# Kernel optimization log

Measured on AMD Instinct MI355X. Metric: run time of the kernel, lower is better.

The kernel has to match this reference:

```python
import jax, jax.numpy as jnp
import numpy as np

N = 100000
E = 1600000
IN_DIM = 128
HID_DIM = 64
OUT_DIM = 1


def setup_inputs() -> dict:
    key = jax.random.key(0)
    k = jax.random.split(key, 8)
    x = jax.random.normal(k[0], (N, IN_DIM), dtype=jnp.float32)
    edge_index = jax.random.randint(k[1], (2, E), 0, N, dtype=jnp.int64)
    # GCNConv glorot-style weights, zero biases
    W1 = jax.random.normal(k[2], (IN_DIM, HID_DIM), dtype=jnp.float32) / np.sqrt(IN_DIM)
    b1 = jnp.zeros((HID_DIM,), dtype=jnp.float32)
    W2 = jax.random.normal(k[3], (HID_DIM, 2), dtype=jnp.float32) / np.sqrt(HID_DIM)
    b2 = jnp.zeros((2,), dtype=jnp.float32)
    Wc = jax.random.normal(k[4], (2, OUT_DIM), dtype=jnp.float32) / np.sqrt(2.0)
    bc = jnp.zeros((OUT_DIM,), dtype=jnp.float32)
    return {"x": x, "edge_index": edge_index, "W1": W1, "b1": b1,
            "W2": W2, "b2": b2, "Wc": Wc, "bc": bc}


def _gcn_conv(x, W, b, row, col, norm, n_nodes):
    """PyG GCNConv: transform, then normalized scatter-add aggregation."""
    h = x @ W                      # [N, out] transform BEFORE propagation
    msgs = h[row] * norm[:, None]  # gather from source nodes, scale
    out = jax.ops.segment_sum(msgs, col, num_segments=n_nodes)  # scatter to targets
    return out + b


def _prep_edges(edge_index, n_nodes):
    # add self-loops (PyG default add_self_loops=True)
    loops = jnp.arange(n_nodes, dtype=edge_index.dtype)
    row = jnp.concatenate([edge_index[0], loops])
    col = jnp.concatenate([edge_index[1], loops])
    # symmetric normalization deg^{-1/2} on both endpoints (edge weight 1)
    deg = jax.ops.segment_sum(jnp.ones_like(col, dtype=jnp.float32), col,
                              num_segments=n_nodes)
    dis = jnp.where(deg > 0, jax.lax.rsqrt(deg), 0.0)
    norm = dis[row] * dis[col]
    return row, col, norm


def reference(x, edge_index, W1, b1, W2, b2, Wc, bc):
    n_nodes = x.shape[0]
    row, col, norm = _prep_edges(edge_index, n_nodes)
    h = jnp.tanh(_gcn_conv(x, W1, b1, row, col, norm, n_nodes))
    emb = jnp.tanh(_gcn_conv(h, W2, b2, row, col, norm, n_nodes))
    return jax.nn.sigmoid(emb @ Wc + bc)  # [N, 1]
```

## Files before the change

### kernel.cpp

```cpp
#include <hip/hip_runtime.h>
#include <math.h>

#define IN_DIM 128
#define HID 64
#define NPB 128
#define NPB_SH 7
#define CAP 4096
#define CHUNK 2048
#define CPT 2

typedef __attribute__((ext_vector_type(8))) short bf16x8;
typedef __attribute__((ext_vector_type(4))) float f32x4;
typedef __attribute__((ext_vector_type(4))) _Float16 f16x4;

static __device__ inline short f2bf(float f) {
    unsigned u = __float_as_uint(f);
    u += 0x7fff + ((u >> 16) & 1);
    return (short)(u >> 16);
}

__device__ __forceinline__ void scanExcl1024(const unsigned* in, unsigned* out,
                                             int m, int t, unsigned* wsum) {
    unsigned v = (t < m) ? in[t] : 0u;
    unsigned incl = v;
    int lane = t & 63;
#pragma unroll
    for (int off = 1; off < 64; off <<= 1) {
        unsigned u = __shfl_up(incl, off, 64);
        if (lane >= off) incl += u;
    }
    if (lane == 63) wsum[t >> 6] = incl;
    __syncthreads();
    if (t < 16) {
        unsigned w = wsum[t];
        unsigned winc = w;
#pragma unroll
        for (int off = 1; off < 16; off <<= 1) {
            unsigned u = __shfl_up(winc, off, 64);
            if (t >= off) winc += u;
        }
        wsum[t] = winc - w;
    }
    __syncthreads();
    if (t < m) out[t] = incl - v + wsum[t >> 6];
}

__global__ void k_packW(const float* __restrict__ W1, ushort* __restrict__ W1p) {
    int idx = blockIdx.x * 256 + threadIdx.x;
    int i = idx & 7, lane = (idx >> 3) & 63, fb = (idx >> 9) & 3, kc = (idx >> 11) & 3;
    int k = kc * 32 + (lane >> 4) * 8 + i;
    int f = fb * 16 + (lane & 15);
    W1p[idx] = (ushort)f2bf(W1[k * HID + f]);
}

__global__ void __launch_bounds__(1024) k_binpairs(
        const int* __restrict__ row, const int* __restrict__ col,
        unsigned* __restrict__ pairsA, unsigned short* __restrict__ chk,
        int E, int nbuk) {
    __shared__ unsigned cntL[1024];
    __shared__ unsigned offs[1024];
    __shared__ unsigned wsum[16];
    __shared__ unsigned stage[CHUNK];
    int t = threadIdx.x;
    int base = blockIdx.x * CHUNK;
    int cc = min(CHUNK, E - base);

    cntL[t] = 0;
    __syncthreads();

    unsigned myPk[CPT], myR[CPT];
    int myB[CPT];
#pragma unroll
    for (int i = 0; i < CPT; ++i) {
        int j = i * 1024 + t;
        myB[i] = -1;
        if (j < cc) {
            int r = row[base + j], c = col[base + j];
            int b = c >> NPB_SH;
            myR[i] = atomicAdd(&cntL[b], 1u);
            myPk[i] = (unsigned)r | ((unsigned)(c & (NPB - 1)) << 24);
            myB[i] = b;
        }
    }
    __syncthreads();
    scanExcl1024(cntL, offs, nbuk, t, wsum);
    __syncthreads();
#pragma unroll
    for (int i = 0; i < CPT; ++i)
        if (myB[i] >= 0) stage[offs[myB[i]] + myR[i]] = myPk[i];
    __syncthreads();
    for (int j = t; j < cc; j += 1024) pairsA[base + j] = stage[j];
    size_t rb = (size_t)blockIdx.x * (nbuk + 1);
    if (t < nbuk) chk[rb + t] = (unsigned short)offs[t];
    if (t == 0) chk[rb + nbuk] = (unsigned short)cc;
}

__global__ void __launch_bounds__(1024) k_sort(
        const unsigned* __restrict__ pairsA, const unsigned short* __restrict__ chk,
        unsigned* __restrict__ pairs2, unsigned* __restrict__ offsG,
        float* __restrict__ dis, int nblk, int nbuk, int n) {
    __shared__ unsigned cntB[1024];
    __shared__ unsigned baseB[1024];
    __shared__ unsigned wsum[16];
    __shared__ unsigned stage[CAP];
    __shared__ unsigned sorted[CAP];
    __shared__ unsigned cntN[NPB];
    __shared__ unsigned offsN[NPB];
    __shared__ unsigned cur[NPB];
    __shared__ unsigned totS;
    int t = threadIdx.x, b = blockIdx.x;

    unsigned s = 0, cntT = 0;
    if (t < nblk) {
        size_t rb = (size_t)t * (nbuk + 1);
        s = chk[rb + b];
        cntT = chk[rb + b + 1] - s;
    }
    cntB[t] = cntT;
    __syncthreads();
    scanExcl1024(cntB, baseB, nblk, t, wsum);
    __syncthreads();
    if (t == 0) totS = baseB[nblk - 1] + cntB[nblk - 1];
    if (t < NPB) cntN[t] = 0;
    if (t < nblk && cntT) {
        unsigned dst = baseB[t];
        const unsigned* sp = pairsA + (size_t)t * CHUNK + s;
        for (unsigned k = 0; k < cntT; ++k)
            if (dst + k < CAP) stage[dst + k] = sp[k];
    }
    __syncthreads();
    int cbt = (int)min(totS, (unsigned)CAP);
    for (int i = t; i < cbt; i += 1024) atomicAdd(&cntN[stage[i] >> 24], 1u);
    __syncthreads();
    scanExcl1024(cntN, offsN, NPB, t, wsum);
    __syncthreads();
    if (t < NPB) cur[t] = offsN[t];
    __syncthreads();
    for (int i = t; i < cbt; i += 1024) {
        unsigned pk = stage[i];
        sorted[atomicAdd(&cur[pk >> 24], 1u)] = pk;
    }
    __syncthreads();
    int cb4 = (cbt + 3) >> 2;
    for (int i = t; i < cb4; i += 1024)
        ((uint4*)(pairs2 + (size_t)b * CAP))[i] = ((const uint4*)sorted)[i];
    if (t <= NPB) offsG[(size_t)b * (NPB + 1) + t] = (t < NPB) ? offsN[t] : (unsigned)cbt;
    int nd = b * NPB + t;
    if (t < NPB && nd < n) dis[nd] = rsqrtf((float)(cntN[t] + 1));
}

__global__ void __launch_bounds__(256) k_gemm1(const float* __restrict__ x,
                                               const ushort* __restrict__ W1p,
                                               const float* __restrict__ dis,
                                               _Float16* __restrict__ h1s, int n) {
    int t = threadIdx.x, wave = t >> 6, lane = t & 63;
    int nb = blockIdx.x * 64 + wave * 16;
    int arow = nb + (lane & 15);
    int g = lane >> 4;
    const bf16x8* Wp = (const bf16x8*)W1p;

    f32x4 acc0 = {0.f, 0.f, 0.f, 0.f}, acc1 = acc0, acc2 = acc0, acc3 = acc0;

#pragma unroll
    for (int kc = 0; kc < 4; ++kc) {
        bf16x8 a;
        if (arow < n) {
            const float4* xp = (const float4*)(x + (size_t)arow * IN_DIM + kc * 32 + g * 8);
            float4 x0 = xp[0], x1 = xp[1];
            a[0] = f2bf(x0.x); a[1] = f2bf(x0.y); a[2] = f2bf(x0.z); a[3] = f2bf(x0.w);
            a[4] = f2bf(x1.x); a[5] = f2bf(x1.y); a[6] = f2bf(x1.z); a[7] = f2bf(x1.w);
        } else {
            for (int i = 0; i < 8; ++i) a[i] = 0;
        }
        acc0 = __builtin_amdgcn_mfma_f32_16x16x32_bf16(a, Wp[(kc * 4 + 0) * 64 + lane], acc0, 0, 0, 0);
        acc1 = __builtin_amdgcn_mfma_f32_16x16x32_bf16(a, Wp[(kc * 4 + 1) * 64 + lane], acc1, 0, 0, 0);
        acc2 = __builtin_amdgcn_mfma_f32_16x16x32_bf16(a, Wp[(kc * 4 + 2) * 64 + lane], acc2, 0, 0, 0);
        acc3 = __builtin_amdgcn_mfma_f32_16x16x32_bf16(a, Wp[(kc * 4 + 3) * 64 + lane], acc3, 0, 0, 0);
    }

    int c = lane & 15, rbase = g * 4;
    float dn[4];
    int nd[4];
#pragma unroll
    for (int r = 0; r < 4; ++r) {
        nd[r] = nb + rbase + r;
        dn[r] = (nd[r] < n) ? dis[nd[r]] : 0.f;
    }
#define EPI(FB, ACC)                                                          \
    {                                                                         \
        int f = FB * 16 + c;                                                  \
        _Pragma("unroll") for (int r = 0; r < 4; ++r) {                       \
            if (nd[r] < n)                                                    \
                h1s[(size_t)nd[r] * HID + f] = (_Float16)(ACC[r] * dn[r]);    \
        }                                                                     \
    }
    EPI(0, acc0) EPI(1, acc1) EPI(2, acc2) EPI(3, acc3)
#undef EPI
}

__global__ void __launch_bounds__(512, 8) k_gather1(
        const unsigned* __restrict__ pairs2, const unsigned* __restrict__ offsG,
        const _Float16* __restrict__ h1s, const float* __restrict__ dis,
        const float* __restrict__ b1, const float* __restrict__ W2,
        float* __restrict__ es, int n) {
    __shared__ unsigned sorted[CAP];
    __shared__ unsigned offs[NPB + 1];
    int t = threadIdx.x, b = blockIdx.x;
    if (t <= NPB) offs[t] = offsG[(size_t)b * (NPB + 1) + t];
    __syncthreads();
    int cbt = (int)offs[NPB];
    int cb4 = (cbt + 3) >> 2;
    for (int i = t; i < cb4; i += 512)
        ((uint4*)sorted)[i] = ((const uint4*)(pairs2 + (size_t)b * CAP))[i];
    __syncthreads();

    int wave = t >> 6, lane = t & 63;
    int grp = lane >> 4, sub = lane & 15;
    float4 bb  = *(const float4*)(b1 + sub * 4);
    float4 w01 = *(const float4*)(W2 + sub * 8);
    float4 w23 = *(const float4*)(W2 + sub * 8 + 4);
    for (int it = 0; it < 16; ++it) {
        int dl = wave * 16 + it;
        int nd = b * NPB + dl;
        if (nd >= n) break;
        int p0 = (int)offs[dl] + grp, p1 = (int)offs[dl + 1];
        float a0 = 0.f, a1 = 0.f, a2 = 0.f, a3 = 0.f;
        for (int pp = p0; pp < p1; pp += 32) {
            f16x4 hacc = {(_Float16)0, (_Float16)0, (_Float16)0, (_Float16)0};
#pragma unroll
            for (int u = 0; u < 8; ++u) {
                int p = pp + u * 4;
                if (p < p1) {
                    unsigned srcn = sorted[p] & 0xFFFFFFu;
                    hacc += *(const f16x4*)(h1s + (size_t)srcn * HID + sub * 4);
                }
            }
            a0 += (float)hacc[0]; a1 += (float)hacc[1];
            a2 += (float)hacc[2]; a3 += (float)hacc[3];
        }
        a0 += __shfl_xor(a0, 16); a0 += __shfl_xor(a0, 32);
        a1 += __shfl_xor(a1, 16); a1 += __shfl_xor(a1, 32);
        a2 += __shfl_xor(a2, 16); a2 += __shfl_xor(a2, 32);
        a3 += __shfl_xor(a3, 16); a3 += __shfl_xor(a3, 32);
        f16x4 sv = *(const f16x4*)(h1s + (size_t)nd * HID + sub * 4);
        a0 += (float)sv[0]; a1 += (float)sv[1]; a2 += (float)sv[2]; a3 += (float)sv[3];
        float d = dis[nd];
        float v0 = tanhf(fmaf(a0, d, bb.x));
        float v1 = tanhf(fmaf(a1, d, bb.y));
        float v2 = tanhf(fmaf(a2, d, bb.z));
        float v3 = tanhf(fmaf(a3, d, bb.w));
        float s0 = v0 * w01.x + v1 * w01.z + v2 * w23.x + v3 * w23.z;
        float s1 = v0 * w01.y + v1 * w01.w + v2 * w23.y + v3 * w23.w;
        s0 += __shfl_xor(s0, 1); s1 += __shfl_xor(s1, 1);
        s0 += __shfl_xor(s0, 2); s1 += __shfl_xor(s1, 2);
        s0 += __shfl_xor(s0, 4); s1 += __shfl_xor(s1, 4);
        s0 += __shfl_xor(s0, 8); s1 += __shfl_xor(s1, 8);
        if (lane == 0) {
            es[nd * 2 + 0] = s0 * d;
            es[nd * 2 + 1] = s1 * d;
        }
    }
}

__global__ void __launch_bounds__(128) k_pass2b(
        const unsigned* __restrict__ pairs2, const unsigned* __restrict__ offsG,
        const float* __restrict__ es, const float* __restrict__ dis,
        const float* __restrict__ b2, const float* __restrict__ Wc,
        const float* __restrict__ bc, float* __restrict__ out, int n) {
    int t = threadIdx.x, b = blockIdx.x;
    int nd = b * NPB + t;
    if (nd >= n) return;
    const unsigned* seg = pairs2 + (size_t)b * CAP;
    int p0 = (int)offsG[(size_t)b * (NPB + 1) + t];
    int p1 = (int)offsG[(size_t)b * (NPB + 1) + t + 1];
    float2 self = *(const float2*)(es + (size_t)nd * 2);
    float a0 = self.x, a1 = self.y;
    for (int p = p0; p < p1; ++p) {
        unsigned srcn = seg[p] & 0xFFFFFFu;
        float2 v = *(const float2*)(es + (size_t)srcn * 2);
        a0 += v.x; a1 += v.y;
    }
    float d = dis[nd];
    float e0 = tanhf(fmaf(a0, d, b2[0]));
    float e1 = tanhf(fmaf(a1, d, b2[1]));
    float z = fmaf(e0, Wc[0], fmaf(e1, Wc[1], bc[0]));
    out[nd] = 1.f / (1.f + expf(-z));
}

extern "C" void kernel_launch(void* const* d_in, const int* in_sizes, int n_in,
                              void* d_out, int out_size, void* d_ws, size_t ws_size,
                              hipStream_t stream) {
    const float* x  = (const float*)d_in[0];
    const int*   ei = (const int*)d_in[1];
    const float* W1 = (const float*)d_in[2];
    const float* b1 = (const float*)d_in[3];
    const float* W2 = (const float*)d_in[4];
    const float* b2 = (const float*)d_in[5];
    const float* Wc = (const float*)d_in[6];
    const float* bc = (const float*)d_in[7];

    const int n = in_sizes[0] / IN_DIM;
    const int E = in_sizes[1] / 2;
    const int* row = ei;
    const int* col = ei + E;
    const int nbuk = (n + NPB - 1) / NPB;
    const int nblk = (E + CHUNK - 1) / CHUNK;

    char* w = (char*)d_ws;
    auto alloc = [&](size_t bytes) {
        char* p = w;
        w += (bytes + 511) & ~(size_t)511;
        return p;
    };
    unsigned*       pairsA = (unsigned*)alloc((size_t)nblk * CHUNK * 4);
    unsigned short* chk    = (unsigned short*)alloc((size_t)nblk * (nbuk + 1) * 2);
    unsigned*       pairs2 = (unsigned*)alloc((size_t)nbuk * CAP * 4);
    unsigned*       offsG  = (unsigned*)alloc((size_t)nbuk * (NPB + 1) * 4);
    float*          dis    = (float*)alloc((size_t)n * 4);
    ushort*         W1p    = (ushort*)alloc(16 * 64 * 8 * 2);
    _Float16*       h1s    = (_Float16*)alloc((size_t)n * HID * 2);
    float*          es     = (float*)alloc((size_t)n * 2 * 4);

    k_packW   <<<32, 256, 0, stream>>>(W1, W1p);
    k_binpairs<<<nblk, 1024, 0, stream>>>(row, col, pairsA, chk, E, nbuk);
    k_sort    <<<nbuk, 1024, 0, stream>>>(pairsA, chk, pairs2, offsG, dis,
                                          nblk, nbuk, n);
    k_gemm1   <<<(n + 63) / 64, 256, 0, stream>>>(x, W1p, dis, h1s, n);
    k_gather1 <<<nbuk, 512, 0, stream>>>(pairs2, offsG, h1s, dis, b1, W2, es, n);
    k_pass2b  <<<nbuk, 128, 0, stream>>>(pairs2, offsG, es, dis, b2, Wc, bc,
                                         (float*)d_out, n);
}
```

Measured before the change: 125.2 us.

## Split gather1 into 64-node blocks and use 16-byte f16x8 row loads

```diff
diff --git a/kernel.cpp b/kernel.cpp
--- a/kernel.cpp
+++ b/kernel.cpp
@@ -12,6 +12,7 @@
 typedef __attribute__((ext_vector_type(8))) short bf16x8;
 typedef __attribute__((ext_vector_type(4))) float f32x4;
 typedef __attribute__((ext_vector_type(4))) _Float16 f16x4;
+typedef __attribute__((ext_vector_type(8))) _Float16 f16x8;
 
 static __device__ inline short f2bf(float f) {
     unsigned u = __float_as_uint(f);
@@ -198,63 +199,86 @@
 #undef EPI
 }
 
-__global__ void __launch_bounds__(512, 8) k_gather1(
+__global__ void __launch_bounds__(256, 8) k_gather1(
         const unsigned* __restrict__ pairs2, const unsigned* __restrict__ offsG,
         const _Float16* __restrict__ h1s, const float* __restrict__ dis,
         const float* __restrict__ b1, const float* __restrict__ W2,
         float* __restrict__ es, int n) {
-    __shared__ unsigned sorted[CAP];
-    __shared__ unsigned offs[NPB + 1];
-    int t = threadIdx.x, b = blockIdx.x;
-    if (t <= NPB) offs[t] = offsG[(size_t)b * (NPB + 1) + t];
-    __syncthreads();
-    int cbt = (int)offs[NPB];
-    int cb4 = (cbt + 3) >> 2;
-    for (int i = t; i < cb4; i += 512)
-        ((uint4*)sorted)[i] = ((const uint4*)(pairs2 + (size_t)b * CAP))[i];
+    __shared__ unsigned sortedL[CAP];
+    __shared__ unsigned offsL[65];
+    int t = threadIdx.x;
+    int nb0 = blockIdx.x * 64;
+    int b = nb0 >> NPB_SH;
+    int dl0 = nb0 & (NPB - 1);
+    if (t <= 64) offsL[t] = offsG[(size_t)b * (NPB + 1) + dl0 + t];
+    __syncthreads();
+    int o0 = (int)offsL[0], o1 = (int)offsL[64];
+    for (int i = t; i < o1 - o0; i += 256)
+        sortedL[i] = pairs2[(size_t)b * CAP + o0 + i];
     __syncthreads();
 
     int wave = t >> 6, lane = t & 63;
-    int grp = lane >> 4, sub = lane & 15;
-    float4 bb  = *(const float4*)(b1 + sub * 4);
-    float4 w01 = *(const float4*)(W2 + sub * 8);
-    float4 w23 = *(const float4*)(W2 + sub * 8 + 4);
+    int grp = lane >> 3, sub = lane & 7;
+    float4 bbA = *(const float4*)(b1 + sub * 8);
+    float4 bbB = *(const float4*)(b1 + sub * 8 + 4);
+    float4 wA = *(const float4*)(W2 + sub * 16);
+    float4 wB = *(const float4*)(W2 + sub * 16 + 4);
+    float4 wC = *(const float4*)(W2 + sub * 16 + 8);
+    float4 wD = *(const float4*)(W2 + sub * 16 + 12);
+
     for (int it = 0; it < 16; ++it) {
         int dl = wave * 16 + it;
-        int nd = b * NPB + dl;
+        int nd = nb0 + dl;
         if (nd >= n) break;
-        int p0 = (int)offs[dl] + grp, p1 = (int)offs[dl + 1];
-        float a0 = 0.f, a1 = 0.f, a2 = 0.f, a3 = 0.f;
+        int p0 = (int)offsL[dl] + grp, p1 = (int)offsL[dl + 1];
+        float a0 = 0.f, a1 = 0.f, a2 = 0.f, a3 = 0.f,
+              a4 = 0.f, a5 = 0.f, a6 = 0.f, a7 = 0.f;
         for (int pp = p0; pp < p1; pp += 32) {
-            f16x4 hacc = {(_Float16)0, (_Float16)0, (_Float16)0, (_Float16)0};
-#pragma unroll
-            for (int u = 0; u < 8; ++u) {
-                int p = pp + u * 4;
+            f16x8 hacc = {0, 0, 0, 0, 0, 0, 0, 0};
+#pragma unroll
+            for (int u = 0; u < 4; ++u) {
+                int p = pp + u * 8;
                 if (p < p1) {
-                    unsigned srcn = sorted[p] & 0xFFFFFFu;
-                    hacc += *(const f16x4*)(h1s + (size_t)srcn * HID + sub * 4);
+                    unsigned srcn = sortedL[p - o0] & 0xFFFFFFu;
+                    hacc += *(const f16x8*)(h1s + (size_t)srcn * HID + sub * 8);
                 }
             }
             a0 += (float)hacc[0]; a1 += (float)hacc[1];
             a2 += (float)hacc[2]; a3 += (float)hacc[3];
-        }
-        a0 += __shfl_xor(a0, 16); a0 += __shfl_xor(a0, 32);
-        a1 += __shfl_xor(a1, 16); a1 += __shfl_xor(a1, 32);
-        a2 += __shfl_xor(a2, 16); a2 += __shfl_xor(a2, 32);
-        a3 += __shfl_xor(a3, 16); a3 += __shfl_xor(a3, 32);
-        f16x4 sv = *(const f16x4*)(h1s + (size_t)nd * HID + sub * 4);
+            a4 += (float)hacc[4]; a5 += (float)hacc[5];
+            a6 += (float)hacc[6]; a7 += (float)hacc[7];
+        }
+        a0 += __shfl_xor(a0, 8);  a1 += __shfl_xor(a1, 8);
+        a2 += __shfl_xor(a2, 8);  a3 += __shfl_xor(a3, 8);
+        a4 += __shfl_xor(a4, 8);  a5 += __shfl_xor(a5, 8);
+        a6 += __shfl_xor(a6, 8);  a7 += __shfl_xor(a7, 8);
+        a0 += __shfl_xor(a0, 16); a1 += __shfl_xor(a1, 16);
+        a2 += __shfl_xor(a2, 16); a3 += __shfl_xor(a3, 16);
+        a4 += __shfl_xor(a4, 16); a5 += __shfl_xor(a5, 16);
+        a6 += __shfl_xor(a6, 16); a7 += __shfl_xor(a7, 16);
+        a0 += __shfl_xor(a0, 32); a1 += __shfl_xor(a1, 32);
+        a2 += __shfl_xor(a2, 32); a3 += __shfl_xor(a3, 32);
+        a4 += __shfl_xor(a4, 32); a5 += __shfl_xor(a5, 32);
+        a6 += __shfl_xor(a6, 32); a7 += __shfl_xor(a7, 32);
+        f16x8 sv = *(const f16x8*)(h1s + (size_t)nd * HID + sub * 8);
         a0 += (float)sv[0]; a1 += (float)sv[1]; a2 += (float)sv[2]; a3 += (float)sv[3];
+        a4 += (float)sv[4]; a5 += (float)sv[5]; a6 += (float)sv[6]; a7 += (float)sv[7];
         float d = dis[nd];
-        float v0 = tanhf(fmaf(a0, d, bb.x));
-        float v1 = tanhf(fmaf(a1, d, bb.y));
-        float v2 = tanhf(fmaf(a2, d, bb.z));
-        float v3 = tanhf(fmaf(a3, d, bb.w));
-        float s0 = v0 * w01.x + v1 * w01.z + v2 * w23.x + v3 * w23.z;
-        float s1 = v0 * w01.y + v1 * w01.w + v2 * w23.y + v3 * w23.w;
+        float v0 = tanhf(fmaf(a0, d, bbA.x));
+        float v1 = tanhf(fmaf(a1, d, bbA.y));
+        float v2 = tanhf(fmaf(a2, d, bbA.z));
+        float v3 = tanhf(fmaf(a3, d, bbA.w));
+        float v4 = tanhf(fmaf(a4, d, bbB.x));
+        float v5 = tanhf(fmaf(a5, d, bbB.y));
+        float v6 = tanhf(fmaf(a6, d, bbB.z));
+        float v7 = tanhf(fmaf(a7, d, bbB.w));
+        float s0 = v0 * wA.x + v1 * wA.z + v2 * wB.x + v3 * wB.z
+                 + v4 * wC.x + v5 * wC.z + v6 * wD.x + v7 * wD.z;
+        float s1 = v0 * wA.y + v1 * wA.w + v2 * wB.y + v3 * wB.w
+                 + v4 * wC.y + v5 * wC.w + v6 * wD.y + v7 * wD.w;
         s0 += __shfl_xor(s0, 1); s1 += __shfl_xor(s1, 1);
         s0 += __shfl_xor(s0, 2); s1 += __shfl_xor(s1, 2);
         s0 += __shfl_xor(s0, 4); s1 += __shfl_xor(s1, 4);
-        s0 += __shfl_xor(s0, 8); s1 += __shfl_xor(s1, 8);
         if (lane == 0) {
             es[nd * 2 + 0] = s0 * d;
             es[nd * 2 + 1] = s1 * d;
@@ -326,7 +350,7 @@
     k_sort    <<<nbuk, 1024, 0, stream>>>(pairsA, chk, pairs2, offsG, dis,
                                           nblk, nbuk, n);
     k_gemm1   <<<(n + 63) / 64, 256, 0, stream>>>(x, W1p, dis, h1s, n);
-    k_gather1 <<<nbuk, 512, 0, stream>>>(pairs2, offsG, h1s, dis, b1, W2, es, n);
+    k_gather1 <<<(n + 63) / 64, 256, 0, stream>>>(pairs2, offsG, h1s, dis, b1, W2, es, n);
     k_pass2b  <<<nbuk, 128, 0, stream>>>(pairs2, offsG, es, dis, b2, Wc, bc,
                                          (float*)d_out, n);
 }
```

New measurement: 128.9 us. 1.03x slower.

## Shrink binning chunks, transpose chunk offsets, and halve gather block granularity

Applied to the files above, without the earlier changes.

```diff
diff --git a/kernel.cpp b/kernel.cpp
--- a/kernel.cpp
+++ b/kernel.cpp
@@ -6,8 +6,8 @@
 #define NPB 128
 #define NPB_SH 7
 #define CAP 4096
-#define CHUNK 2048
-#define CPT 2
+#define CHUNK 1024
+#define SLDS 2048
 
 typedef __attribute__((ext_vector_type(8))) short bf16x8;
 typedef __attribute__((ext_vector_type(4))) float f32x4;
@@ -17,32 +17,6 @@
     unsigned u = __float_as_uint(f);
     u += 0x7fff + ((u >> 16) & 1);
     return (short)(u >> 16);
-}
-
-__device__ __forceinline__ void scanExcl1024(const unsigned* in, unsigned* out,
-                                             int m, int t, unsigned* wsum) {
-    unsigned v = (t < m) ? in[t] : 0u;
-    unsigned incl = v;
-    int lane = t & 63;
-#pragma unroll
-    for (int off = 1; off < 64; off <<= 1) {
-        unsigned u = __shfl_up(incl, off, 64);
-        if (lane >= off) incl += u;
-    }
-    if (lane == 63) wsum[t >> 6] = incl;
-    __syncthreads();
-    if (t < 16) {
-        unsigned w = wsum[t];
-        unsigned winc = w;
-#pragma unroll
-        for (int off = 1; off < 16; off <<= 1) {
-            unsigned u = __shfl_up(winc, off, 64);
-            if (t >= off) winc += u;
-        }
-        wsum[t] = winc - w;
-    }
-    __syncthreads();
-    if (t < m) out[t] = incl - v + wsum[t >> 6];
 }
 
 __global__ void k_packW(const float* __restrict__ W1, ushort* __restrict__ W1p) {
@@ -53,26 +27,26 @@
     W1p[idx] = (ushort)f2bf(W1[k * HID + f]);
 }
 
-__global__ void __launch_bounds__(1024) k_binpairs(
+__global__ void __launch_bounds__(256) k_binpairs(
         const int* __restrict__ row, const int* __restrict__ col,
         unsigned* __restrict__ pairsA, unsigned short* __restrict__ chk,
         int E, int nbuk) {
     __shared__ unsigned cntL[1024];
     __shared__ unsigned offs[1024];
-    __shared__ unsigned wsum[16];
+    __shared__ unsigned wsum[4];
     __shared__ unsigned stage[CHUNK];
     int t = threadIdx.x;
     int base = blockIdx.x * CHUNK;
     int cc = min(CHUNK, E - base);
 
-    cntL[t] = 0;
-    __syncthreads();
-
-    unsigned myPk[CPT], myR[CPT];
-    int myB[CPT];
-#pragma unroll
-    for (int i = 0; i < CPT; ++i) {
-        int j = i * 1024 + t;
+    for (int i = t; i < nbuk; i += 256) cntL[i] = 0;
+    __syncthreads();
+
+    unsigned myPk[4], myR[4];
+    int myB[4];
+#pragma unroll
+    for (int i = 0; i < 4; ++i) {
+        int j = i * 256 + t;
         myB[i] = -1;
         if (j < cc) {
             int r = row[base + j], c = col[base + j];
@@ -83,66 +57,149 @@
         }
     }
     __syncthreads();
-    scanExcl1024(cntL, offs, nbuk, t, wsum);
-    __syncthreads();
-#pragma unroll
-    for (int i = 0; i < CPT; ++i)
+    unsigned cb[4];
+#pragma unroll
+    for (int k = 0; k < 4; ++k) {
+        int bb = 4 * t + k;
+        cb[k] = (bb < nbuk) ? cntL[bb] : 0u;
+    }
+    unsigned s = cb[0] + cb[1] + cb[2] + cb[3];
+    unsigned incl = s;
+    int lane = t & 63;
+#pragma unroll
+    for (int off = 1; off < 64; off <<= 1) {
+        unsigned u = __shfl_up(incl, off, 64);
+        if (lane >= off) incl += u;
+    }
+    if (lane == 63) wsum[t >> 6] = incl;
+    __syncthreads();
+    if (t == 0) {
+        unsigned a = 0;
+        for (int i = 0; i < 4; ++i) { unsigned v = wsum[i]; wsum[i] = a; a += v; }
+    }
+    __syncthreads();
+    unsigned bs = incl - s + wsum[t >> 6];
+#pragma unroll
+    for (int k = 0; k < 4; ++k) {
+        int bb = 4 * t + k;
+        if (bb < nbuk) offs[bb] = bs;
+        bs += cb[k];
+    }
+    __syncthreads();
+#pragma unroll
+    for (int i = 0; i < 4; ++i)
         if (myB[i] >= 0) stage[offs[myB[i]] + myR[i]] = myPk[i];
     __syncthreads();
-    for (int j = t; j < cc; j += 1024) pairsA[base + j] = stage[j];
+    if (cc == CHUNK) {
+        ((uint4*)(pairsA + base))[t] = ((const uint4*)stage)[t];
+    } else {
+        for (int j = t; j < cc; j += 256) pairsA[base + j] = stage[j];
+    }
     size_t rb = (size_t)blockIdx.x * (nbuk + 1);
-    if (t < nbuk) chk[rb + t] = (unsigned short)offs[t];
-    if (t == 0) chk[rb + nbuk] = (unsigned short)cc;
-}
-
-__global__ void __launch_bounds__(1024) k_sort(
-        const unsigned* __restrict__ pairsA, const unsigned short* __restrict__ chk,
+    for (int i = t; i <= nbuk; i += 256)
+        chk[rb + i] = (unsigned short)((i < nbuk) ? offs[i] : (unsigned)cc);
+}
+
+__global__ void __launch_bounds__(256) k_tr(const unsigned short* __restrict__ chk,
+                                            unsigned short* __restrict__ chkT,
+                                            int nblk, int nbukR, int nblkP) {
+    __shared__ unsigned short tile[32][33];
+    int r0 = blockIdx.x * 32, c0 = blockIdx.y * 32;
+    int tx = threadIdx.x & 31, ty = threadIdx.x >> 5;
+#pragma unroll
+    for (int k = 0; k < 4; ++k) {
+        int r = r0 + ty + k * 8, c = c0 + tx;
+        if (r < nblk && c < nbukR) tile[ty + k * 8][tx] = chk[(size_t)r * nbukR + c];
+    }
+    __syncthreads();
+#pragma unroll
+    for (int k = 0; k < 4; ++k) {
+        int c = c0 + ty + k * 8, r = r0 + tx;
+        if (c < nbukR && r < nblk) chkT[(size_t)c * nblkP + r] = tile[tx][ty + k * 8];
+    }
+}
+
+__global__ void __launch_bounds__(512) k_sort(
+        const unsigned* __restrict__ pairsA, const unsigned short* __restrict__ chkT,
         unsigned* __restrict__ pairs2, unsigned* __restrict__ offsG,
-        float* __restrict__ dis, int nblk, int nbuk, int n) {
-    __shared__ unsigned cntB[1024];
-    __shared__ unsigned baseB[1024];
-    __shared__ unsigned wsum[16];
+        float* __restrict__ dis, int nblk, int nblkP, int nbuk, int n) {
     __shared__ unsigned stage[CAP];
     __shared__ unsigned sorted[CAP];
     __shared__ unsigned cntN[NPB];
     __shared__ unsigned offsN[NPB];
     __shared__ unsigned cur[NPB];
+    __shared__ unsigned wsum[8];
     __shared__ unsigned totS;
     int t = threadIdx.x, b = blockIdx.x;
-
-    unsigned s = 0, cntT = 0;
-    if (t < nblk) {
-        size_t rb = (size_t)t * (nbuk + 1);
-        s = chk[rb + b];
-        cntT = chk[rb + b + 1] - s;
-    }
-    cntB[t] = cntT;
-    __syncthreads();
-    scanExcl1024(cntB, baseB, nblk, t, wsum);
-    __syncthreads();
-    if (t == 0) totS = baseB[nblk - 1] + cntB[nblk - 1];
+    const unsigned short* r0 = chkT + (size_t)b * nblkP;
+    const unsigned short* r1 = r0 + nblkP;
+
+    unsigned st[4], ct[4];
+#pragma unroll
+    for (int k = 0; k < 4; ++k) {
+        int ch = 4 * t + k;
+        if (ch < nblk) {
+            st[k] = r0[ch];
+            ct[k] = (unsigned)r1[ch] - st[k];
+        } else { st[k] = 0; ct[k] = 0; }
+    }
+    unsigned s = ct[0] + ct[1] + ct[2] + ct[3];
+    unsigned incl = s;
+    int lane = t & 63;
+#pragma unroll
+    for (int off = 1; off < 64; off <<= 1) {
+        unsigned u = __shfl_up(incl, off, 64);
+        if (lane >= off) incl += u;
+    }
+    if (lane == 63) wsum[t >> 6] = incl;
+    __syncthreads();
+    if (t == 0) {
+        unsigned a = 0;
+        for (int i = 0; i < 8; ++i) { unsigned v = wsum[i]; wsum[i] = a; a += v; }
+        totS = a;
+    }
     if (t < NPB) cntN[t] = 0;
-    if (t < nblk && cntT) {
-        unsigned dst = baseB[t];
-        const unsigned* sp = pairsA + (size_t)t * CHUNK + s;
-        for (unsigned k = 0; k < cntT; ++k)
-            if (dst + k < CAP) stage[dst + k] = sp[k];
+    __syncthreads();
+    unsigned bs = incl - s + wsum[t >> 6];
+#pragma unroll
+    for (int k = 0; k < 4; ++k) {
+        if (ct[k]) {
+            const unsigned* sp = pairsA + (size_t)(4 * t + k) * CHUNK + st[k];
+            for (unsigned u = 0; u < ct[k]; ++u)
+                if (bs + u < CAP) stage[bs + u] = sp[u];
+        }
+        bs += ct[k];
     }
     __syncthreads();
     int cbt = (int)min(totS, (unsigned)CAP);
-    for (int i = t; i < cbt; i += 1024) atomicAdd(&cntN[stage[i] >> 24], 1u);
-    __syncthreads();
-    scanExcl1024(cntN, offsN, NPB, t, wsum);
-    __syncthreads();
-    if (t < NPB) cur[t] = offsN[t];
-    __syncthreads();
-    for (int i = t; i < cbt; i += 1024) {
+    for (int i = t; i < cbt; i += 512) atomicAdd(&cntN[stage[i] >> 24], 1u);
+    __syncthreads();
+    if (t < NPB) {
+        unsigned c = cntN[t], in2 = c;
+#pragma unroll
+        for (int off = 1; off < 64; off <<= 1) {
+            unsigned u = __shfl_up(in2, off, 64);
+            if (lane >= off) in2 += u;
+        }
+        if (lane == 63) wsum[t >> 6] = in2;
+        offsN[t] = in2 - c;
+    }
+    __syncthreads();
+    if (t == 0) { unsigned a = wsum[0]; wsum[0] = 0; wsum[1] = a; }
+    __syncthreads();
+    if (t < NPB) {
+        unsigned o = offsN[t] + wsum[t >> 6];
+        offsN[t] = o;
+        cur[t] = o;
+    }
+    __syncthreads();
+    for (int i = t; i < cbt; i += 512) {
         unsigned pk = stage[i];
         sorted[atomicAdd(&cur[pk >> 24], 1u)] = pk;
     }
     __syncthreads();
     int cb4 = (cbt + 3) >> 2;
-    for (int i = t; i < cb4; i += 1024)
+    for (int i = t; i < cb4; i += 512)
         ((uint4*)(pairs2 + (size_t)b * CAP))[i] = ((const uint4*)sorted)[i];
     if (t <= NPB) offsG[(size_t)b * (NPB + 1) + t] = (t < NPB) ? offsN[t] : (unsigned)cbt;
     int nd = b * NPB + t;
@@ -198,20 +255,23 @@
 #undef EPI
 }
 
-__global__ void __launch_bounds__(512, 8) k_gather1(
+__global__ void __launch_bounds__(512) k_gather1(
         const unsigned* __restrict__ pairs2, const unsigned* __restrict__ offsG,
         const _Float16* __restrict__ h1s, const float* __restrict__ dis,
         const float* __restrict__ b1, const float* __restrict__ W2,
         float* __restrict__ es, int n) {
-    __shared__ unsigned sorted[CAP];
-    __shared__ unsigned offs[NPB + 1];
-    int t = threadIdx.x, b = blockIdx.x;
-    if (t <= NPB) offs[t] = offsG[(size_t)b * (NPB + 1) + t];
-    __syncthreads();
-    int cbt = (int)offs[NPB];
-    int cb4 = (cbt + 3) >> 2;
-    for (int i = t; i < cb4; i += 512)
-        ((uint4*)sorted)[i] = ((const uint4*)(pairs2 + (size_t)b * CAP))[i];
+    __shared__ unsigned sortedL[SLDS];
+    __shared__ unsigned offsL[65];
+    int t = threadIdx.x;
+    int nb0 = blockIdx.x * 64;
+    int b = nb0 >> NPB_SH;
+    int dl0 = nb0 & (NPB - 1);
+    if (t <= 64) offsL[t] = offsG[(size_t)b * (NPB + 1) + dl0 + t];
+    __syncthreads();
+    int o0 = (int)offsL[0], o1 = (int)offsL[64];
+    int len = o1 - o0;
+    const unsigned* gseg = pairs2 + (size_t)b * CAP;
+    for (int i = t; i < len && i < SLDS; i += 512) sortedL[i] = gseg[o0 + i];
     __syncthreads();
 
     int wave = t >> 6, lane = t & 63;
@@ -219,47 +279,50 @@
     float4 bb  = *(const float4*)(b1 + sub * 4);
     float4 w01 = *(const float4*)(W2 + sub * 8);
     float4 w23 = *(const float4*)(W2 + sub * 8 + 4);
-    for (int it = 0; it < 16; ++it) {
-        int dl = wave * 16 + it;
-        int nd = b * NPB + dl;
-        if (nd >= n) break;
-        int p0 = (int)offs[dl] + grp, p1 = (int)offs[dl + 1];
-        float a0 = 0.f, a1 = 0.f, a2 = 0.f, a3 = 0.f;
-        for (int pp = p0; pp < p1; pp += 32) {
-            f16x4 hacc = {(_Float16)0, (_Float16)0, (_Float16)0, (_Float16)0};
-#pragma unroll
-            for (int u = 0; u < 8; ++u) {
-                int p = pp + u * 4;
-                if (p < p1) {
-                    unsigned srcn = sorted[p] & 0xFFFFFFu;
-                    hacc += *(const f16x4*)(h1s + (size_t)srcn * HID + sub * 4);
-                }
-            }
-            a0 += (float)hacc[0]; a1 += (float)hacc[1];
-            a2 += (float)hacc[2]; a3 += (float)hacc[3];
-        }
-        a0 += __shfl_xor(a0, 16); a0 += __shfl_xor(a0, 32);
-        a1 += __shfl_xor(a1, 16); a1 += __shfl_xor(a1, 32);
-        a2 += __shfl_xor(a2, 16); a2 += __shfl_xor(a2, 32);
-        a3 += __shfl_xor(a3, 16); a3 += __shfl_xor(a3, 32);
-        f16x4 sv = *(const f16x4*)(h1s + (size_t)nd * HID + sub * 4);
-        a0 += (float)sv[0]; a1 += (float)sv[1]; a2 += (float)sv[2]; a3 += (float)sv[3];
-        float d = dis[nd];
-        float v0 = tanhf(fmaf(a0, d, bb.x));
-        float v1 = tanhf(fmaf(a1, d, bb.y));
-        float v2 = tanhf(fmaf(a2, d, bb.z));
-        float v3 = tanhf(fmaf(a3, d, bb.w));
-        float s0 = v0 * w01.x + v1 * w01.z + v2 * w23.x + v3 * w23.z;
-        float s1 = v0 * w01.y + v1 * w01.w + v2 * w23.y + v3 * w23.w;
-        s0 += __shfl_xor(s0, 1); s1 += __shfl_xor(s1, 1);
-        s0 += __shfl_xor(s0, 2); s1 += __shfl_xor(s1, 2);
-        s0 += __shfl_xor(s0, 4); s1 += __shfl_xor(s1, 4);
-        s0 += __shfl_xor(s0, 8); s1 += __shfl_xor(s1, 8);
-        if (lane == 0) {
-            es[nd * 2 + 0] = s0 * d;
-            es[nd * 2 + 1] = s1 * d;
-        }
-    }
+
+#define GBODY(FETCH)                                                           \
+    for (int it = 0; it < 8; ++it) {                                           \
+        int dl = wave * 8 + it;                                                \
+        int nd = nb0 + dl;                                                     \
+        if (nd >= n) break;                                                    \
+        int p0 = (int)offsL[dl] + grp, p1 = (int)offsL[dl + 1];                \
+        float a0 = 0.f, a1 = 0.f, a2 = 0.f, a3 = 0.f;                          \
+        for (int p = p0; p < p1; p += 4) {                                     \
+            unsigned srcn = (FETCH) & 0xFFFFFFu;                               \
+            f16x4 v = *(const f16x4*)(h1s + (size_t)srcn * HID + sub * 4);     \
+            a0 += (float)v[0]; a1 += (float)v[1];                              \
+            a2 += (float)v[2]; a3 += (float)v[3];                              \
+        }                                                                      \
+        a0 += __shfl_xor(a0, 16); a0 += __shfl_xor(a0, 32);                    \
+        a1 += __shfl_xor(a1, 16); a1 += __shfl_xor(a1, 32);                    \
+        a2 += __shfl_xor(a2, 16); a2 += __shfl_xor(a2, 32);                    \
+        a3 += __shfl_xor(a3, 16); a3 += __shfl_xor(a3, 32);                    \
+        f16x4 sv = *(const f16x4*)(h1s + (size_t)nd * HID + sub * 4);          \
+        a0 += (float)sv[0]; a1 += (float)sv[1];                                \
+        a2 += (float)sv[2]; a3 += (float)sv[3];                                \
+        float d = dis[nd];                                                     \
+        float v0 = tanhf(fmaf(a0, d, bb.x));                                   \
+        float v1 = tanhf(fmaf(a1, d, bb.y));                                   \
+        float v2 = tanhf(fmaf(a2, d, bb.z));                                   \
+        float v3 = tanhf(fmaf(a3, d, bb.w));                                   \
+        float s0 = v0 * w01.x + v1 * w01.z + v2 * w23.x + v3 * w23.z;          \
+        float s1 = v0 * w01.y + v1 * w01.w + v2 * w23.y + v3 * w23.w;          \
+        s0 += __shfl_xor(s0, 1); s1 += __shfl_xor(s1, 1);                      \
+        s0 += __shfl_xor(s0, 2); s1 += __shfl_xor(s1, 2);                      \
+        s0 += __shfl_xor(s0, 4); s1 += __shfl_xor(s1, 4);                      \
+        s0 += __shfl_xor(s0, 8); s1 += __shfl_xor(s1, 8);                      \
+        if (lane == 0) {                                                       \
+            es[nd * 2 + 0] = s0 * d;                                           \
+            es[nd * 2 + 1] = s1 * d;                                           \
+        }                                                                      \
+    }
+
+    if (len <= SLDS) {
+        GBODY(sortedL[p - o0])
+    } else {
+        GBODY(gseg[p])
+    }
+#undef GBODY
 }
 
 __global__ void __launch_bounds__(128) k_pass2b(
@@ -304,7 +367,9 @@
     const int* row = ei;
     const int* col = ei + E;
     const int nbuk = (n + NPB - 1) / NPB;
+    const int nbukR = nbuk + 1;
     const int nblk = (E + CHUNK - 1) / CHUNK;
+    const int nblkP = (nblk + 3) & ~3;
 
     char* w = (char*)d_ws;
     auto alloc = [&](size_t bytes) {
@@ -313,7 +378,8 @@
         return p;
     };
     unsigned*       pairsA = (unsigned*)alloc((size_t)nblk * CHUNK * 4);
-    unsigned short* chk    = (unsigned short*)alloc((size_t)nblk * (nbuk + 1) * 2);
+    unsigned short* chk    = (unsigned short*)alloc((size_t)nblk * nbukR * 2);
+    unsigned short* chkT   = (unsigned short*)alloc((size_t)nbukR * nblkP * 2);
     unsigned*       pairs2 = (unsigned*)alloc((size_t)nbuk * CAP * 4);
     unsigned*       offsG  = (unsigned*)alloc((size_t)nbuk * (NPB + 1) * 4);
     float*          dis    = (float*)alloc((size_t)n * 4);
@@ -322,11 +388,15 @@
     float*          es     = (float*)alloc((size_t)n * 2 * 4);
 
     k_packW   <<<32, 256, 0, stream>>>(W1, W1p);
-    k_binpairs<<<nblk, 1024, 0, stream>>>(row, col, pairsA, chk, E, nbuk);
-    k_sort    <<<nbuk, 1024, 0, stream>>>(pairsA, chk, pairs2, offsG, dis,
-                                          nblk, nbuk, n);
+    k_binpairs<<<nblk, 256, 0, stream>>>(row, col, pairsA, chk, E, nbuk);
+    {
+        dim3 g((nblk + 31) / 32, (nbukR + 31) / 32);
+        k_tr<<<g, 256, 0, stream>>>(chk, chkT, nblk, nbukR, nblkP);
+    }
+    k_sort    <<<nbuk, 512, 0, stream>>>(pairsA, chkT, pairs2, offsG, dis,
+                                         nblk, nblkP, nbuk, n);
     k_gemm1   <<<(n + 63) / 64, 256, 0, stream>>>(x, W1p, dis, h1s, n);
-    k_gather1 <<<nbuk, 512, 0, stream>>>(pairs2, offsG, h1s, dis, b1, W2, es, n);
+    k_gather1 <<<(n + 63) / 64, 512, 0, stream>>>(pairs2, offsG, h1s, dis, b1, W2, es, n);
     k_pass2b  <<<nbuk, 128, 0, stream>>>(pairs2, offsG, es, dis, b2, Wc, bc,
                                          (float*)d_out, n);
 }
```

Result: faster. 119.3 us (-4.7%).
